# Kernel tuning notes

Hardware: AMD Instinct MI355X
Metric: run time of the kernel (lower is better)

The kernel has to match this reference:

```python
import jax, jax.numpy as jnp
import numpy as np

NUM_HEADS = 6
TAU = 1.0


def _split_heads(y, h):
    b, n, c = y.shape
    return y.reshape(b, n, h, c // h).transpose(0, 2, 1, 3)  # b h n d


def setup_inputs() -> dict:
    key = jax.random.key(0)
    B, M, C = 8, 1026, 384
    names = ["Wq1", "Wq2", "Wk1", "Wk2", "Wv1", "Wv2", "Wo"]
    ks = jax.random.split(key, len(names) + 3)
    inp = {"x": jax.random.normal(ks[0], (B, M, C), jnp.float32)}
    for i, nm in enumerate(names):
        inp[nm] = jax.random.normal(ks[i + 1], (C, C), jnp.float32) * 0.02
        inp["b" + nm[1:]] = jnp.zeros((C,), jnp.float32)
    inp["weights"] = jax.random.normal(ks[-2], (4,), jnp.float32)
    u = jax.random.uniform(ks[-1], (4,), jnp.float32, 1e-6, 1.0 - 1e-6)
    inp["gumbel_noise"] = -jnp.log(-jnp.log(u))  # fixed gumbel sample for determinism
    return inp


def reference(x, Wq1, bq1, Wq2, bq2, Wk1, bk1, Wk2, bk2,
              Wv1, bv1, Wv2, bv2, Wo, bo, weights, gumbel_noise):
    B, M, C = x.shape
    N1 = (M - 2) // 2 + 1  # N + 1, quadrant size
    h = NUM_HEADS
    d = C // h
    scale = d ** -0.5
    x1, x2 = x[:, :N1], x[:, N1:]
    q = jnp.concatenate([_split_heads(x1 @ Wq1 + bq1, h),
                         _split_heads(x2 @ Wq2 + bq2, h)], axis=2)  # b h M d
    k = jnp.concatenate([_split_heads(x1 @ Wk1 + bk1, h),
                         _split_heads(x2 @ Wk2 + bk2, h)], axis=2)
    v1 = _split_heads(x1 @ Wv1 + bv1, h)  # b h N1 d
    v2 = _split_heads(x2 @ Wv2 + bv2, h)
    attn = jnp.einsum('bhqd,bhkd->bhqk', q, k) * scale  # b h M M
    b1 = jax.nn.softmax(attn[:, :, :N1, :N1], axis=-1)
    b2 = jax.nn.softmax(attn[:, :, :N1, N1:], axis=-1)
    b3 = jax.nn.softmax(attn[:, :, N1:, :N1], axis=-1)
    b4 = jax.nn.softmax(attn[:, :, N1:, N1:], axis=-1)
    # hard gumbel-softmax gate (straight-through)
    y_soft = jax.nn.softmax((weights + gumbel_noise) / TAU)
    y_hard = jax.nn.one_hot(jnp.argmax(y_soft), 4, dtype=y_soft.dtype)
    w = y_hard + y_soft - jax.lax.stop_gradient(y_soft)
    A = w[0] * b1 + w[1] * b2 + w[2] * b3 + w[3] * b4  # b h N1 N1
    out1 = jnp.einsum('bhqk,bhkd->bhqd', A, v1)
    out2 = jnp.einsum('bhqk,bhkd->bhqd', A, v2)
    out = jnp.concatenate([out1, out2], axis=2)  # b h M d
    out = out.transpose(0, 2, 1, 3).reshape(B, M, C)
    return out @ Wo + bo
```

## Files before the change

### kernel.cpp

```cpp
#include <hip/hip_runtime.h>

typedef unsigned short u16;
typedef short v8s __attribute__((ext_vector_type(8)));
typedef float v4f __attribute__((ext_vector_type(4)));

namespace {
constexpr int kC = 384;
constexpr int kN1 = 513;
constexpr int kH = 6;
constexpr int kBH = 48;
constexpr int kRows = 4104;
constexpr int kRows2 = 8208;
constexpr int kPld = 576;
constexpr int kTotX = 8208 * 384;
}

#if __has_builtin(__builtin_amdgcn_exp2f)
#define EXP2F(x) __builtin_amdgcn_exp2f(x)
#else
#define EXP2F(x) exp2f(x)
#endif

__device__ __forceinline__ u16 f2b(float f) {
  unsigned int u = __float_as_uint(f);
  u += 0x7fffu + ((u >> 16) & 1u);
  return (u16)(u >> 16);
}

__device__ __forceinline__ int gumbel_argmax(const float* __restrict__ w,
                                             const float* __restrict__ g) {
  float v0 = w[0] + g[0], v1 = w[1] + g[1], v2 = w[2] + g[2], v3 = w[3] + g[3];
  int j = 0;
  float m = v0;
  if (v1 > m) { m = v1; j = 1; }
  if (v2 > m) { m = v2; j = 2; }
  if (v3 > m) { m = v3; j = 3; }
  return j;
}

__global__ __launch_bounds__(256) void prep_w(
    const float* __restrict__ Wq1, const float* __restrict__ Wq2,
    const float* __restrict__ Wk1, const float* __restrict__ Wk2,
    const float* __restrict__ Wv1, const float* __restrict__ Wv2,
    const float* __restrict__ Wo, const float* __restrict__ x,
    const float* __restrict__ wts, const float* __restrict__ gum,
    u16* __restrict__ Wqt, u16* __restrict__ Wkt, u16* __restrict__ Wv1t,
    u16* __restrict__ Wv2t, u16* __restrict__ Wot, u16* __restrict__ xb) {
  const int bx = blockIdx.x;
  if (bx >= 720) {
    const int base = (bx - 720) * 4096 + (int)threadIdx.x * 8;
    for (int p = 0; p < 2; ++p) {
      const int idx = base + p * 2048;
      if (idx < kTotX) {
        const float4 f0 = *(const float4*)(x + idx);
        const float4 f1 = *(const float4*)(x + idx + 4);
        const v8s v = {(short)f2b(f0.x), (short)f2b(f0.y), (short)f2b(f0.z),
                       (short)f2b(f0.w), (short)f2b(f1.x), (short)f2b(f1.y),
                       (short)f2b(f1.z), (short)f2b(f1.w)};
        *(v8s*)(xb + idx) = v;
      }
    }
    return;
  }
  __shared__ float tb[32][33];
  const int z = bx / 144, rem = bx - z * 144;
  const int c0 = (rem % 12) * 32, r0 = (rem / 12) * 32;
  const int j = gumbel_argmax(wts, gum);
  const float* src;
  u16* dst;
  switch (z) {
    case 0: src = (j < 2) ? Wq1 : Wq2; dst = Wqt; break;
    case 1: src = (j == 0 || j == 2) ? Wk1 : Wk2; dst = Wkt; break;
    case 2: src = Wv1; dst = Wv1t; break;
    case 3: src = Wv2; dst = Wv2t; break;
    default: src = Wo; dst = Wot; break;
  }
  const int tx = threadIdx.x & 31, ty = threadIdx.x >> 5;
  for (int p = 0; p < 4; ++p)
    tb[ty + p * 8][tx] = src[(size_t)(r0 + ty + p * 8) * kC + c0 + tx];
  __syncthreads();
  for (int p = 0; p < 4; ++p)
    dst[(size_t)(c0 + ty + p * 8) * kC + r0 + tx] = f2b(tb[tx][ty + p * 8]);
}

__global__ __launch_bounds__(256) void qkv_mfma(
    const u16* __restrict__ xb, const u16* __restrict__ Wqt,
    const u16* __restrict__ Wkt, const u16* __restrict__ Wv1t,
    const u16* __restrict__ Wv2t, const float* __restrict__ bq1,
    const float* __restrict__ bq2, const float* __restrict__ bk1,
    const float* __restrict__ bk2, const float* __restrict__ bv1,
    const float* __restrict__ bv2, const float* __restrict__ wts,
    const float* __restrict__ gum, u16* __restrict__ Qb, u16* __restrict__ Kb,
    u16* __restrict__ Vt1, u16* __restrict__ Vt2) {
  const int bid = blockIdx.x;
  const int xcd = bid & 7;
  const int op = xcd >> 1;
  const int wu = (bid >> 3) * 2 + (xcd & 1);
  if (wu >= 99) return;
  const int mb33 = wu / 3, nb3 = wu - mb33 * 3;

  __shared__ __align__(16) u16 As[128][72];
  __shared__ __align__(16) u16 Bs[128][72];
  const int j = gumbel_argmax(wts, gum);
  const bool vmode = (op >= 2);
  const float* bias;
  int xoff;
  const u16* Wt;
  if (op == 0) {
    bias = (j < 2) ? bq1 : bq2; xoff = (j < 2) ? 0 : kN1; Wt = Wqt;
  } else if (op == 1) {
    const bool u1 = (j == 0 || j == 2);
    bias = u1 ? bk1 : bk2; xoff = u1 ? 0 : kN1; Wt = Wkt;
  } else if (op == 2) {
    bias = bv1; xoff = 0; Wt = Wv1t;
  } else {
    bias = bv2; xoff = kN1; Wt = Wv2t;
  }
  const int m0 = (vmode ? nb3 : mb33) * 128;
  const int n0 = (vmode ? mb33 : nb3) * 128;
  const int tid = threadIdx.x;
  const int lane = tid & 63, l16 = lane & 15, quad = lane >> 4;
  const int wv = tid >> 6, wr = wv >> 1, wc = wv & 1;
  const int sr = tid >> 2, sc = (tid & 3) * 16;

  v4f acc[4][4];
  const v4f z4 = {0.f, 0.f, 0.f, 0.f};
  for (int i = 0; i < 4; ++i)
    for (int n = 0; n < 4; ++n) acc[i][n] = z4;

  for (int k0 = 0; k0 < kC; k0 += 64) {
    for (int p = 0; p < 2; ++p) {
      const int r = p * 64 + sr;
      v8s v0 = {0, 0, 0, 0, 0, 0, 0, 0}, v1 = v0;
      if (!vmode) {
        const int t = m0 + r;
        if (t < kRows) {
          const int bb = t / kN1, mm = t - bb * kN1;
          const u16* s = xb + ((size_t)(bb * 1026 + xoff + mm)) * kC + k0 + sc;
          v0 = *(const v8s*)s;
          v1 = *(const v8s*)(s + 8);
        }
      } else {
        const u16* s = Wt + (size_t)(m0 + r) * kC + k0 + sc;
        v0 = *(const v8s*)s;
        v1 = *(const v8s*)(s + 8);
      }
      *(v8s*)&As[r][sc] = v0;
      *(v8s*)&As[r][sc + 8] = v1;
    }
    for (int p = 0; p < 2; ++p) {
      const int r = p * 64 + sr;
      v8s v0 = {0, 0, 0, 0, 0, 0, 0, 0}, v1 = v0;
      if (!vmode) {
        const u16* s = Wt + (size_t)(n0 + r) * kC + k0 + sc;
        v0 = *(const v8s*)s;
        v1 = *(const v8s*)(s + 8);
      } else {
        const int t = n0 + r;
        if (t < kRows) {
          const int bb = t / kN1, mm = t - bb * kN1;
          const u16* s = xb + ((size_t)(bb * 1026 + xoff + mm)) * kC + k0 + sc;
          v0 = *(const v8s*)s;
          v1 = *(const v8s*)(s + 8);
        }
      }
      *(v8s*)&Bs[r][sc] = v0;
      *(v8s*)&Bs[r][sc + 8] = v1;
    }
    __syncthreads();
    for (int ks = 0; ks < 2; ++ks) {
      v8s af[4], bfr[4];
      for (int i = 0; i < 4; ++i)
        af[i] = *(const v8s*)&As[wr * 64 + i * 16 + l16][ks * 32 + quad * 8];
      for (int n = 0; n < 4; ++n)
        bfr[n] = *(const v8s*)&Bs[wc * 64 + n * 16 + l16][ks * 32 + quad * 8];
      for (int i = 0; i < 4; ++i)
        for (int n = 0; n < 4; ++n)
          acc[i][n] = __builtin_amdgcn_mfma_f32_16x16x32_bf16(af[i], bfr[n],
                                                              acc[i][n], 0, 0, 0);
    }
    __syncthreads();
  }

  if (!vmode) {
    u16* outp = (op == 0) ? Qb : Kb;
    const float osc = (op == 0) ? 0.18033688011112042f : 1.0f;
    float bv4[4];
    for (int nt = 0; nt < 4; ++nt) bv4[nt] = bias[n0 + wc * 64 + nt * 16 + l16];
    for (int i = 0; i < 4; ++i) {
      const int rowb = m0 + wr * 64 + i * 16 + quad * 4;
      for (int r = 0; r < 4; ++r) {
        const int row = rowb + r;
        if (row >= kRows) continue;
        for (int nt = 0; nt < 4; ++nt) {
          const int col = n0 + wc * 64 + nt * 16 + l16;
          outp[(size_t)row * kC + col] = f2b((acc[i][nt][r] + bv4[nt]) * osc);
        }
      }
    }
  } else {
    u16* Vt = (op == 2) ? Vt1 : Vt2;
    for (int nt = 0; nt < 4; ++nt) {
      const int t = n0 + wc * 64 + nt * 16 + l16;
      if (t >= kRows) continue;
      const int bb = t / kN1, mm = t - bb * kN1;
      for (int i = 0; i < 4; ++i) {
        const int colb = m0 + wr * 64 + i * 16 + quad * 4;
        for (int r = 0; r < 4; ++r) {
          const int col = colb + r;
          const int hh = col >> 6, d = col & 63;
          Vt[((size_t)(bb * kH + hh) * 64 + d) * kPld + mm] =
              f2b(acc[i][nt][r] + bias[col]);
        }
      }
    }
  }
}

__global__ __launch_bounds__(256) void attn_fused(const u16* __restrict__ Qb,
                                                  const u16* __restrict__ Kb,
                                                  const u16* __restrict__ Vt1,
                                                  const u16* __restrict__ Vt2,
                                                  u16* __restrict__ PRE) {
  __shared__ __align__(16) u16 Ks[64][72];
  __shared__ __align__(16) u16 Vs[128][72];
  __shared__ __align__(16) u16 Ps[4][16][72];
  const int bid = blockIdx.x;
  const int xcd = bid & 7;
  const int t6 = bid >> 3;
  const int bh = xcd * 6 + (t6 % 6);
  const int q0 = (t6 / 6) * 64;
  const int b = bh / kH, hh = bh - b * kH;
  const int tid = threadIdx.x;
  const int w = tid >> 6, lane = tid & 63, l16 = lane & 15, quad = lane >> 4;
  v8s aq0, aq1;
  {
    int qr = q0 + w * 16 + l16;
    if (qr > 512) qr = 512;
    const u16* qs = Qb + ((size_t)(b * kN1 + qr)) * kC + hh * 64 + quad * 8;
    aq0 = *(const v8s*)qs;
    aq1 = *(const v8s*)(qs + 32);
  }
  const int ksr = tid >> 2, ksc = (tid & 3) * 16;
  const int vd = tid >> 1, vc = (tid & 1) * 32;
  const u16* kbase = Kb + (size_t)b * kN1 * kC + hh * 64 + ksc;
  const u16* vbase = ((vd < 64) ? (Vt1 + ((size_t)bh * 64 + vd) * kPld)
                                : (Vt2 + ((size_t)bh * 64 + (vd - 64)) * kPld)) +
                     vc;
  v8s kr0, kr1, vr0, vr1, vr2, vr3;
  {
    const u16* s = kbase + (size_t)ksr * kC;
    kr0 = *(const v8s*)s;
    kr1 = *(const v8s*)(s + 8);
    vr0 = *(const v8s*)(vbase);
    vr1 = *(const v8s*)(vbase + 8);
    vr2 = *(const v8s*)(vbase + 16);
    vr3 = *(const v8s*)(vbase + 24);
  }
  float lsum[4] = {0.f, 0.f, 0.f, 0.f};
  v4f Oacc[8];
  const v4f z4 = {0.f, 0.f, 0.f, 0.f};
  for (int n = 0; n < 8; ++n) Oacc[n] = z4;

  for (int kt = 0; kt < 9; ++kt) {
    const int k0 = kt * 64;
    __syncthreads();
    *(v8s*)&Ks[ksr][ksc] = kr0;
    *(v8s*)&Ks[ksr][ksc + 8] = kr1;
    *(v8s*)&Vs[vd][vc] = vr0;
    *(v8s*)&Vs[vd][vc + 8] = vr1;
    *(v8s*)&Vs[vd][vc + 16] = vr2;
    *(v8s*)&Vs[vd][vc + 24] = vr3;
    __syncthreads();
    if (kt < 8) {
      int ki = k0 + 64 + ksr;
      if (ki > 512) ki = 512;
      const u16* s = kbase + (size_t)ki * kC;
      kr0 = *(const v8s*)s;
      kr1 = *(const v8s*)(s + 8);
      const u16* t = vbase + k0 + 64;
      vr0 = *(const v8s*)t;
      vr1 = *(const v8s*)(t + 8);
      vr2 = *(const v8s*)(t + 16);
      vr3 = *(const v8s*)(t + 24);
    }
    v4f sacc[4];
    for (int nt = 0; nt < 4; ++nt) sacc[nt] = z4;
    for (int nt = 0; nt < 4; ++nt) {
      const v8s bk0 = *(const v8s*)&Ks[nt * 16 + l16][quad * 8];
      sacc[nt] = __builtin_amdgcn_mfma_f32_16x16x32_bf16(aq0, bk0, sacc[nt], 0, 0, 0);
      const v8s bk1 = *(const v8s*)&Ks[nt * 16 + l16][32 + quad * 8];
      sacc[nt] = __builtin_amdgcn_mfma_f32_16x16x32_bf16(aq1, bk1, sacc[nt], 0, 0, 0);
    }
    if (kt < 8) {
      for (int r = 0; r < 4; ++r) {
        float ps = 0.f;
        for (int nt = 0; nt < 4; ++nt) {
          const float p = EXP2F(sacc[nt][r]);
          ps += p;
          Ps[w][quad * 4 + r][nt * 16 + l16] = f2b(p);
        }
        lsum[r] += ps;
      }
    } else {
      for (int r = 0; r < 4; ++r) {
        float ps = 0.f;
        for (int nt = 0; nt < 4; ++nt) {
          const int col = k0 + nt * 16 + l16;
          const float p = (col < kN1) ? EXP2F(sacc[nt][r]) : 0.f;
          ps += p;
          Ps[w][quad * 4 + r][nt * 16 + l16] = f2b(p);
        }
        lsum[r] += ps;
      }
    }
    for (int kc = 0; kc < 2; ++kc) {
      const v8s ap = *(const v8s*)&Ps[w][l16][kc * 32 + quad * 8];
      for (int n = 0; n < 8; ++n) {
        const v8s bv = *(const v8s*)&Vs[n * 16 + l16][kc * 32 + quad * 8];
        Oacc[n] = __builtin_amdgcn_mfma_f32_16x16x32_bf16(ap, bv, Oacc[n], 0, 0, 0);
      }
    }
  }
  float rinv[4];
  for (int r = 0; r < 4; ++r) {
    float s = lsum[r];
    for (int o = 1; o <= 8; o <<= 1) s += __shfl_xor(s, o);
    rinv[r] = 1.f / s;
  }
  for (int n = 0; n < 8; ++n) {
    const int col = hh * 64 + (n & 3) * 16 + l16;
    const int rbase = b * 1026 + ((n < 4) ? 0 : kN1);
    for (int r = 0; r < 4; ++r) {
      const int q = q0 + w * 16 + quad * 4 + r;
      if (q >= kN1) continue;
      PRE[(size_t)(rbase + q) * kC + col] = f2b(Oacc[n][r] * rinv[r]);
    }
  }
}

__global__ __launch_bounds__(256) void out_mfma(const u16* __restrict__ PRE,
                                                const u16* __restrict__ Wot,
                                                const float* __restrict__ bo,
                                                float* __restrict__ OUT) {
  __shared__ __align__(16) u16 As[128][72];
  __shared__ __align__(16) u16 Bs[128][72];
  const int m0 = blockIdx.x * 128, n0 = blockIdx.y * 128;
  const int tid = threadIdx.x;
  const int lane = tid & 63, l16 = lane & 15, quad = lane >> 4;
  const int wv = tid >> 6, wr = wv >> 1, wc = wv & 1;
  const int sr = tid >> 2, sc = (tid & 3) * 16;
  v4f acc[4][4];
  const v4f z4 = {0.f, 0.f, 0.f, 0.f};
  for (int i = 0; i < 4; ++i)
    for (int n = 0; n < 4; ++n) acc[i][n] = z4;
  for (int k0 = 0; k0 < kC; k0 += 64) {
    for (int p = 0; p < 2; ++p) {
      const int r = p * 64 + sr;
      v8s v0 = {0, 0, 0, 0, 0, 0, 0, 0}, v1 = v0;
      const int row = m0 + r;
      if (row < kRows2) {
        const u16* s = PRE + (size_t)row * kC + k0 + sc;
        v0 = *(const v8s*)s;
        v1 = *(const v8s*)(s + 8);
      }
      *(v8s*)&As[r][sc] = v0;
      *(v8s*)&As[r][sc + 8] = v1;
      const u16* s2 = Wot + (size_t)(n0 + r) * kC + k0 + sc;
      *(v8s*)&Bs[r][sc] = *(const v8s*)s2;
      *(v8s*)&Bs[r][sc + 8] = *(const v8s*)(s2 + 8);
    }
    __syncthreads();
    for (int ks = 0; ks < 2; ++ks) {
      v8s af[4], bfr[4];
      for (int i = 0; i < 4; ++i)
        af[i] = *(const v8s*)&As[wr * 64 + i * 16 + l16][ks * 32 + quad * 8];
      for (int n = 0; n < 4; ++n)
        bfr[n] = *(const v8s*)&Bs[wc * 64 + n * 16 + l16][ks * 32 + quad * 8];
      for (int i = 0; i < 4; ++i)
        for (int n = 0; n < 4; ++n)
          acc[i][n] = __builtin_amdgcn_mfma_f32_16x16x32_bf16(af[i], bfr[n],
                                                              acc[i][n], 0, 0, 0);
    }
    __syncthreads();
  }
  float bv4[4];
  for (int nt = 0; nt < 4; ++nt) bv4[nt] = bo[n0 + wc * 64 + nt * 16 + l16];
  for (int i = 0; i < 4; ++i) {
    const int rowb = m0 + wr * 64 + i * 16 + quad * 4;
    for (int r = 0; r < 4; ++r) {
      const int row = rowb + r;
      if (row >= kRows2) continue;
      for (int nt = 0; nt < 4; ++nt) {
        const int col = n0 + wc * 64 + nt * 16 + l16;
        OUT[(size_t)row * kC + col] = acc[i][nt][r] + bv4[nt];
      }
    }
  }
}

extern "C" void kernel_launch(void* const* d_in, const int* in_sizes, int n_in,
                              void* d_out, int out_size, void* d_ws,
                              size_t ws_size, hipStream_t stream) {
  const float* x = (const float*)d_in[0];
  const float* Wq1 = (const float*)d_in[1];
  const float* bq1 = (const float*)d_in[2];
  const float* Wq2 = (const float*)d_in[3];
  const float* bq2 = (const float*)d_in[4];
  const float* Wk1 = (const float*)d_in[5];
  const float* bk1 = (const float*)d_in[6];
  const float* Wk2 = (const float*)d_in[7];
  const float* bk2 = (const float*)d_in[8];
  const float* Wv1 = (const float*)d_in[9];
  const float* bv1 = (const float*)d_in[10];
  const float* Wv2 = (const float*)d_in[11];
  const float* bv2 = (const float*)d_in[12];
  const float* Wo = (const float*)d_in[13];
  const float* bo = (const float*)d_in[14];
  const float* wts = (const float*)d_in[15];
  const float* gum = (const float*)d_in[16];
  (void)Wo;

  u16* Wqt = (u16*)d_ws;
  u16* Wkt = Wqt + 147456;
  u16* Wv1t = Wkt + 147456;
  u16* Wv2t = Wv1t + 147456;
  u16* Wot = Wv2t + 147456;
  u16* Qb = Wot + 147456;
  u16* Kb = Qb + (size_t)kRows * kC;
  u16* Vt1 = Kb + (size_t)kRows * kC;
  u16* Vt2 = Vt1 + (size_t)kBH * 64 * kPld;
  u16* PRE = Vt2 + (size_t)kBH * 64 * kPld;
  u16* XB = PRE + (size_t)kRows2 * kC;

  prep_w<<<dim3(1490), 256, 0, stream>>>(Wq1, Wq2, Wk1, Wk2, Wv1, Wv2, Wo, x,
                                         wts, gum, Wqt, Wkt, Wv1t, Wv2t, Wot,
                                         XB);
  qkv_mfma<<<dim3(400), 256, 0, stream>>>(
      XB, Wqt, Wkt, Wv1t, Wv2t, bq1, bq2, bk1, bk2, bv1, bv2, wts, gum, Qb, Kb,
      Vt1, Vt2);
  attn_fused<<<dim3(432), 256, 0, stream>>>(Qb, Kb, Vt1, Vt2, PRE);
  out_mfma<<<dim3(65, 3), 256, 0, stream>>>(PRE, Wot, bo, (float*)d_out);
}
```

Baseline: 148.2 us.

## Register-prefetch next K tile in GEMMs and peel last attention key column

The projection and output GEMMs now load the next K-slice of global data into registers while MFMAs run on the current shared tile, and drop one barrier per iteration. The attention kernel no longer runs a ninth 64-wide key tile to cover key 512. That single key is handled as a scalar epilogue: a dot product reduced by shuffles, then a rank-1 update of the output. This avoids mostly-masked MFMA work, at the cost of more registers held for prefetch and somewhat delicate shuffle logic in the epilogue.

New measurement: 139.4 us. -5.9%, faster.

```diff
diff --git a/kernel.cpp b/kernel.cpp
--- a/kernel.cpp
+++ b/kernel.cpp
@@ -25,6 +25,10 @@
   unsigned int u = __float_as_uint(f);
   u += 0x7fffu + ((u >> 16) & 1u);
   return (u16)(u >> 16);
+}
+
+__device__ __forceinline__ float b2f(u16 b) {
+  return __uint_as_float(((unsigned)b) << 16);
 }
 
 __device__ __forceinline__ int gumbel_argmax(const float* __restrict__ w,
@@ -128,46 +132,65 @@
   for (int i = 0; i < 4; ++i)
     for (int n = 0; n < 4; ++n) acc[i][n] = z4;
 
+  const v8s z8 = {0, 0, 0, 0, 0, 0, 0, 0};
+  auto prefA = [&](int k0v, int p, v8s& o0, v8s& o1) {
+    const int r = p * 64 + sr;
+    o0 = z8; o1 = z8;
+    if (!vmode) {
+      const int t = m0 + r;
+      if (t < kRows) {
+        const int bb = t / kN1, mm = t - bb * kN1;
+        const u16* s = xb + ((size_t)(bb * 1026 + xoff + mm)) * kC + k0v + sc;
+        o0 = *(const v8s*)s;
+        o1 = *(const v8s*)(s + 8);
+      }
+    } else {
+      const u16* s = Wt + (size_t)(m0 + r) * kC + k0v + sc;
+      o0 = *(const v8s*)s;
+      o1 = *(const v8s*)(s + 8);
+    }
+  };
+  auto prefB = [&](int k0v, int p, v8s& o0, v8s& o1) {
+    const int r = p * 64 + sr;
+    o0 = z8; o1 = z8;
+    if (!vmode) {
+      const u16* s = Wt + (size_t)(n0 + r) * kC + k0v + sc;
+      o0 = *(const v8s*)s;
+      o1 = *(const v8s*)(s + 8);
+    } else {
+      const int t = n0 + r;
+      if (t < kRows) {
+        const int bb = t / kN1, mm = t - bb * kN1;
+        const u16* s = xb + ((size_t)(bb * 1026 + xoff + mm)) * kC + k0v + sc;
+        o0 = *(const v8s*)s;
+        o1 = *(const v8s*)(s + 8);
+      }
+    }
+  };
+
+  v8s a00, a01, a10, a11, b00, b01, b10, b11;
+  prefA(0, 0, a00, a01);
+  prefA(0, 1, a10, a11);
+  prefB(0, 0, b00, b01);
+  prefB(0, 1, b10, b11);
+
   for (int k0 = 0; k0 < kC; k0 += 64) {
-    for (int p = 0; p < 2; ++p) {
-      const int r = p * 64 + sr;
-      v8s v0 = {0, 0, 0, 0, 0, 0, 0, 0}, v1 = v0;
-      if (!vmode) {
-        const int t = m0 + r;
-        if (t < kRows) {
-          const int bb = t / kN1, mm = t - bb * kN1;
-          const u16* s = xb + ((size_t)(bb * 1026 + xoff + mm)) * kC + k0 + sc;
-          v0 = *(const v8s*)s;
-          v1 = *(const v8s*)(s + 8);
-        }
-      } else {
-        const u16* s = Wt + (size_t)(m0 + r) * kC + k0 + sc;
-        v0 = *(const v8s*)s;
-        v1 = *(const v8s*)(s + 8);
-      }
-      *(v8s*)&As[r][sc] = v0;
-      *(v8s*)&As[r][sc + 8] = v1;
-    }
-    for (int p = 0; p < 2; ++p) {
-      const int r = p * 64 + sr;
-      v8s v0 = {0, 0, 0, 0, 0, 0, 0, 0}, v1 = v0;
-      if (!vmode) {
-        const u16* s = Wt + (size_t)(n0 + r) * kC + k0 + sc;
-        v0 = *(const v8s*)s;
-        v1 = *(const v8s*)(s + 8);
-      } else {
-        const int t = n0 + r;
-        if (t < kRows) {
-          const int bb = t / kN1, mm = t - bb * kN1;
-          const u16* s = xb + ((size_t)(bb * 1026 + xoff + mm)) * kC + k0 + sc;
-          v0 = *(const v8s*)s;
-          v1 = *(const v8s*)(s + 8);
-        }
-      }
-      *(v8s*)&Bs[r][sc] = v0;
-      *(v8s*)&Bs[r][sc + 8] = v1;
-    }
+    if (k0) __syncthreads();
+    *(v8s*)&As[sr][sc] = a00;
+    *(v8s*)&As[sr][sc + 8] = a01;
+    *(v8s*)&As[64 + sr][sc] = a10;
+    *(v8s*)&As[64 + sr][sc + 8] = a11;
+    *(v8s*)&Bs[sr][sc] = b00;
+    *(v8s*)&Bs[sr][sc + 8] = b01;
+    *(v8s*)&Bs[64 + sr][sc] = b10;
+    *(v8s*)&Bs[64 + sr][sc + 8] = b11;
     __syncthreads();
+    if (k0 + 64 < kC) {
+      prefA(k0 + 64, 0, a00, a01);
+      prefA(k0 + 64, 1, a10, a11);
+      prefB(k0 + 64, 0, b00, b01);
+      prefB(k0 + 64, 1, b10, b11);
+    }
     for (int ks = 0; ks < 2; ++ks) {
       v8s af[4], bfr[4];
       for (int i = 0; i < 4; ++i)
@@ -179,7 +202,6 @@
           acc[i][n] = __builtin_amdgcn_mfma_f32_16x16x32_bf16(af[i], bfr[n],
                                                               acc[i][n], 0, 0, 0);
     }
-    __syncthreads();
   }
 
   if (!vmode) {
@@ -262,7 +284,7 @@
   const v4f z4 = {0.f, 0.f, 0.f, 0.f};
   for (int n = 0; n < 8; ++n) Oacc[n] = z4;
 
-  for (int kt = 0; kt < 9; ++kt) {
+  for (int kt = 0; kt < 8; ++kt) {
     const int k0 = kt * 64;
     __syncthreads();
     *(v8s*)&Ks[ksr][ksc] = kr0;
@@ -272,10 +294,8 @@
     *(v8s*)&Vs[vd][vc + 16] = vr2;
     *(v8s*)&Vs[vd][vc + 24] = vr3;
     __syncthreads();
-    if (kt < 8) {
-      int ki = k0 + 64 + ksr;
-      if (ki > 512) ki = 512;
-      const u16* s = kbase + (size_t)ki * kC;
+    if (kt < 7) {
+      const u16* s = kbase + (size_t)(k0 + 64 + ksr) * kC;
       kr0 = *(const v8s*)s;
       kr1 = *(const v8s*)(s + 8);
       const u16* t = vbase + k0 + 64;
@@ -292,27 +312,14 @@
       const v8s bk1 = *(const v8s*)&Ks[nt * 16 + l16][32 + quad * 8];
       sacc[nt] = __builtin_amdgcn_mfma_f32_16x16x32_bf16(aq1, bk1, sacc[nt], 0, 0, 0);
     }
-    if (kt < 8) {
-      for (int r = 0; r < 4; ++r) {
-        float ps = 0.f;
-        for (int nt = 0; nt < 4; ++nt) {
-          const float p = EXP2F(sacc[nt][r]);
-          ps += p;
-          Ps[w][quad * 4 + r][nt * 16 + l16] = f2b(p);
-        }
-        lsum[r] += ps;
-      }
-    } else {
-      for (int r = 0; r < 4; ++r) {
-        float ps = 0.f;
-        for (int nt = 0; nt < 4; ++nt) {
-          const int col = k0 + nt * 16 + l16;
-          const float p = (col < kN1) ? EXP2F(sacc[nt][r]) : 0.f;
-          ps += p;
-          Ps[w][quad * 4 + r][nt * 16 + l16] = f2b(p);
-        }
-        lsum[r] += ps;
-      }
+    for (int r = 0; r < 4; ++r) {
+      float ps = 0.f;
+      for (int nt = 0; nt < 4; ++nt) {
+        const float p = EXP2F(sacc[nt][r]);
+        ps += p;
+        Ps[w][quad * 4 + r][nt * 16 + l16] = f2b(p);
+      }
+      lsum[r] += ps;
     }
     for (int kc = 0; kc < 2; ++kc) {
       const v8s ap = *(const v8s*)&Ps[w][l16][kc * 32 + quad * 8];
@@ -322,6 +329,31 @@
       }
     }
   }
+
+  {
+    const u16* k512 = Kb + ((size_t)(b * kN1 + 512)) * kC + hh * 64 + quad * 8;
+    const v8s kv0 = *(const v8s*)k512;
+    const v8s kv1 = *(const v8s*)(k512 + 32);
+    float part = 0.f;
+    for (int jj = 0; jj < 8; ++jj) {
+      part += b2f((u16)aq0[jj]) * b2f((u16)kv0[jj]);
+      part += b2f((u16)aq1[jj]) * b2f((u16)kv1[jj]);
+    }
+    part += __shfl_xor(part, 16);
+    part += __shfl_xor(part, 32);
+    const float p512 = EXP2F(part);
+    float pb[4];
+    for (int r = 0; r < 4; ++r) pb[r] = __shfl(p512, quad * 4 + r);
+    for (int r = 0; r < 4; ++r) lsum[r] += pb[r] * 0.0625f;
+    for (int n = 0; n < 8; ++n) {
+      const int d = (n & 3) * 16 + l16;
+      const u16* vp = (n < 4) ? (Vt1 + ((size_t)bh * 64 + d) * kPld + 512)
+                              : (Vt2 + ((size_t)bh * 64 + d) * kPld + 512);
+      const float vv = b2f(*vp);
+      for (int r = 0; r < 4; ++r) Oacc[n][r] += pb[r] * vv;
+    }
+  }
+
   float rinv[4];
   for (int r = 0; r < 4; ++r) {
     float s = lsum[r];
@@ -354,23 +386,47 @@
   const v4f z4 = {0.f, 0.f, 0.f, 0.f};
   for (int i = 0; i < 4; ++i)
     for (int n = 0; n < 4; ++n) acc[i][n] = z4;
+
+  const v8s z8 = {0, 0, 0, 0, 0, 0, 0, 0};
+  auto lA = [&](int k0v, int p, v8s& o0, v8s& o1) {
+    const int r = p * 64 + sr;
+    o0 = z8; o1 = z8;
+    const int row = m0 + r;
+    if (row < kRows2) {
+      const u16* s = PRE + (size_t)row * kC + k0v + sc;
+      o0 = *(const v8s*)s;
+      o1 = *(const v8s*)(s + 8);
+    }
+  };
+  auto lB = [&](int k0v, int p, v8s& o0, v8s& o1) {
+    const u16* s2 = Wot + (size_t)(n0 + p * 64 + sr) * kC + k0v + sc;
+    o0 = *(const v8s*)s2;
+    o1 = *(const v8s*)(s2 + 8);
+  };
+
+  v8s a00, a01, a10, a11, b00, b01, b10, b11;
+  lA(0, 0, a00, a01);
+  lA(0, 1, a10, a11);
+  lB(0, 0, b00, b01);
+  lB(0, 1, b10, b11);
+
   for (int k0 = 0; k0 < kC; k0 += 64) {
-    for (int p = 0; p < 2; ++p) {
-      const int r = p * 64 + sr;
-      v8s v0 = {0, 0, 0, 0, 0, 0, 0, 0}, v1 = v0;
-      const int row = m0 + r;
-      if (row < kRows2) {
-        const u16* s = PRE + (size_t)row * kC + k0 + sc;
-        v0 = *(const v8s*)s;
-        v1 = *(const v8s*)(s + 8);
-      }
-      *(v8s*)&As[r][sc] = v0;
-      *(v8s*)&As[r][sc + 8] = v1;
-      const u16* s2 = Wot + (size_t)(n0 + r) * kC + k0 + sc;
-      *(v8s*)&Bs[r][sc] = *(const v8s*)s2;
-      *(v8s*)&Bs[r][sc + 8] = *(const v8s*)(s2 + 8);
-    }
+    if (k0) __syncthreads();
+    *(v8s*)&As[sr][sc] = a00;
+    *(v8s*)&As[sr][sc + 8] = a01;
+    *(v8s*)&As[64 + sr][sc] = a10;
+    *(v8s*)&As[64 + sr][sc + 8] = a11;
+    *(v8s*)&Bs[sr][sc] = b00;
+    *(v8s*)&Bs[sr][sc + 8] = b01;
+    *(v8s*)&Bs[64 + sr][sc] = b10;
+    *(v8s*)&Bs[64 + sr][sc + 8] = b11;
     __syncthreads();
+    if (k0 + 64 < kC) {
+      lA(k0 + 64, 0, a00, a01);
+      lA(k0 + 64, 1, a10, a11);
+      lB(k0 + 64, 0, b00, b01);
+      lB(k0 + 64, 1, b10, b11);
+    }
     for (int ks = 0; ks < 2; ++ks) {
       v8s af[4], bfr[4];
       for (int i = 0; i < 4; ++i)
@@ -382,7 +438,6 @@
           acc[i][n] = __builtin_amdgcn_mfma_f32_16x16x32_bf16(af[i], bfr[n],
                                                               acc[i][n], 0, 0, 0);
     }
-    __syncthreads();
   }
   float bv4[4];
   for (int nt = 0; nt < 4; ++nt) bv4[nt] = bo[n0 + wc * 64 + nt * 16 + l16];
```
